# Kernel tuning notes

Measured on AMD Instinct MI355X. Metric: run time of the kernel, lower is better.

## Reference

```python
import jax, jax.numpy as jnp
import numpy as np

EMB = 512
HID = 512
NCLASS = 50257
BATCH = 64
STEPS = 256


def setup_inputs() -> dict:
    key = jax.random.key(0)
    ks = jax.random.split(key, 14)
    s_e = 1.0 / np.sqrt(EMB)
    s_h = 1.0 / np.sqrt(HID)
    inp = {
        "X": jax.random.randint(ks[0], (BATCH, STEPS), 0, NCLASS, dtype=jnp.int32),
        "emb": jax.random.normal(ks[1], (NCLASS, EMB), jnp.float32) * 0.02,
        # layer 1: gates concatenated in order [i, f, g, o]
        "Wi": jax.random.normal(ks[2], (EMB, 4 * HID), jnp.float32) * s_e,
        "Wh": jax.random.normal(ks[3], (HID, 4 * HID), jnp.float32) * s_h,
        "bi": jax.random.normal(ks[4], (4 * HID,), jnp.float32) * 0.01,
        "bh": jax.random.normal(ks[5], (4 * HID,), jnp.float32) * 0.01,
        # layer 2 (computed but unused for the output, as in the original)
        "Wi1": jax.random.normal(ks[6], (HID, 4 * HID), jnp.float32) * s_h,
        "Wh1": jax.random.normal(ks[7], (HID, 4 * HID), jnp.float32) * s_h,
        "bi1": jax.random.normal(ks[8], (4 * HID,), jnp.float32) * 0.01,
        "bh1": jax.random.normal(ks[9], (4 * HID,), jnp.float32) * 0.01,
        # output projection (nn.Linear(n_hidden, n_class, bias=False) => W: [n_class, n_hidden])
        "Wout": jax.random.normal(ks[10], (NCLASS, HID), jnp.float32) * s_h,
        "bout": jnp.ones((NCLASS,), jnp.float32),
    }
    return inp


def _gates(pre):
    i, f, g, o = jnp.split(pre, 4, axis=-1)
    return jax.nn.sigmoid(i), jax.nn.sigmoid(f), jnp.tanh(g), jax.nn.sigmoid(o)


def reference(X, emb, Wi, Wh, bi, bh, Wi1, Wh1, bi1, bh1, Wout, bout):
    x = emb[X]  # [B, T, E]
    B = x.shape[0]
    # precompute input projections for layer 1 for all timesteps: [T, B, 4H]
    xw = jnp.einsum("bte,eh->tbh", x, Wi) + bi + bh

    h0 = jnp.zeros((B, HID), x.dtype)
    carry0 = (h0, h0, h0, h0)  # h, c, h1, c1

    def step(carry, xw_t):
        h, c, h1, c1 = carry
        i, f, g, o = _gates(xw_t + h @ Wh)
        c = f * c + i * g
        h = o * jnp.tanh(c)
        i1, f1, g1, o1 = _gates(h @ Wi1 + bi1 + h1 @ Wh1 + bh1)
        c1 = f1 * c1 + i1 * g1
        h1 = o1 * jnp.tanh(c1)
        return (h, c, h1, c1), None

    (h, c, h1, c1), _ = jax.lax.scan(step, carry0, xw)
    # original: outputs[-1] is layer-1 h at the last timestep
    return h @ Wout.T + bout
```

## Files before the change

### kernel.cpp

```cpp
#include <hip/hip_runtime.h>
#include <cstdint>
#include <cstddef>

#define EMB    512
#define HID    512
#define NCLASS 50257
#define BATCH  64
#define STEPS  256
#define FOURH  2048
#define NBLK   64

typedef __attribute__((ext_vector_type(8))) short    bf16x8;
typedef __attribute__((ext_vector_type(4))) float    f32x4;
typedef __attribute__((ext_vector_type(8))) _Float16 h8v;

__device__ __forceinline__ unsigned short f2bf(float f) {
    union { float f; unsigned int u; } v; v.f = f;
    unsigned int u = v.u;
    return (unsigned short)((u + 0x7fffu + ((u >> 16) & 1u)) >> 16);
}


__global__ void k_bias(const float* __restrict__ bi, const float* __restrict__ bh,
                       float* __restrict__ bias) {
    int i = blockIdx.x * 256 + threadIdx.x;
    if (i < FOURH) bias[i] = bi[i] + bh[i];
}

__global__ void k_wit(const float* __restrict__ Wi, unsigned short* __restrict__ WiT) {
    int n = blockIdx.x;
    int l = threadIdx.x;
    int k0 = l * 8;
    unsigned short t[8];
#pragma unroll
    for (int i = 0; i < 8; i++)
        t[i] = f2bf(Wi[(size_t)(k0 + i) * FOURH + n]);
    uint4 v;
    v.x = (unsigned)t[0] | ((unsigned)t[1] << 16);
    v.y = (unsigned)t[2] | ((unsigned)t[3] << 16);
    v.z = (unsigned)t[4] | ((unsigned)t[5] << 16);
    v.w = (unsigned)t[6] | ((unsigned)t[7] << 16);
    *(uint4*)(WiT + (size_t)n * EMB + k0) = v;
}

__global__ void k_whP(const float* __restrict__ Wh, _Float16* __restrict__ WhP) {
    int idx = blockIdx.x;
    int bidb = idx >> 5, c = idx & 31;
    int ul   = ((c >> 4) << 2) + ((c >> 2) & 3);
    int gate = c & 3;
    int gcol = gate * 512 + bidb * 8 + ul;
    int k0 = threadIdx.x * 8;
    h8v r;
#pragma unroll
    for (int i = 0; i < 8; i++)
        r[i] = (_Float16)Wh[(size_t)(k0 + i) * FOURH + gcol];
    *(h8v*)(WhP + (size_t)idx * 512 + k0) = r;
}

__global__ void k_gather(const int* __restrict__ X, const float* __restrict__ emb,
                         unsigned short* __restrict__ XA) {
    int chunk = blockIdx.x * 256 + threadIdx.x;
    int m  = chunk >> 6;
    int c8 = (chunk & 63) * 8;
    int t = m >> 6, b = m & 63;
    int row = X[b * STEPS + t];
    const float4* src = (const float4*)(emb + (size_t)row * EMB + c8);
    float4 f0 = src[0], f1 = src[1];
    uint4 v;
    v.x = (unsigned)f2bf(f0.x) | ((unsigned)f2bf(f0.y) << 16);
    v.y = (unsigned)f2bf(f0.z) | ((unsigned)f2bf(f0.w) << 16);
    v.z = (unsigned)f2bf(f1.x) | ((unsigned)f2bf(f1.y) << 16);
    v.w = (unsigned)f2bf(f1.z) | ((unsigned)f2bf(f1.w) << 16);
    *(uint4*)(XA + (size_t)m * EMB + c8) = v;
}

__global__ void k_zero(int* __restrict__ p, int n) {
    int i = blockIdx.x * 256 + threadIdx.x;
    if (i < n) p[i] = 0;
}

__global__ __launch_bounds__(256) void k_gemm1(const unsigned short* __restrict__ XA,
                                               const unsigned short* __restrict__ WiT,
                                               const float* __restrict__ bias,
                                               float* __restrict__ XWT) {
    __shared__ unsigned short Al[64 * 48];
    __shared__ unsigned short Bl[64 * 48];
    const int t  = blockIdx.y;
    const int m0 = t * 64;
    const int n0 = blockIdx.x * 64;
    const int tid  = threadIdx.x;
    const int w    = tid >> 6;
    const int lane = tid & 63;
    const int quad = lane >> 4;
    const int l16  = lane & 15;
    const int ar = tid >> 2;
    const int ac = (tid & 3) * 8;

    f32x4 acc[4];
#pragma unroll
    for (int i = 0; i < 4; i++) acc[i] = (f32x4){0.f, 0.f, 0.f, 0.f};

    for (int kk = 0; kk < 16; kk++) {
        const int k0 = kk * 32;
        __syncthreads();
        *(uint4*)(&Al[ar * 48 + ac]) = *(const uint4*)(XA  + (size_t)(m0 + ar) * EMB + k0 + ac);
        *(uint4*)(&Bl[ar * 48 + ac]) = *(const uint4*)(WiT + (size_t)(n0 + ar) * EMB + k0 + ac);
        __syncthreads();
        bf16x8 afrag = *(const bf16x8*)(&Bl[(w * 16 + l16) * 48 + quad * 8]);
#pragma unroll
        for (int mt = 0; mt < 4; mt++) {
            bf16x8 bfrag = *(const bf16x8*)(&Al[(mt * 16 + l16) * 48 + quad * 8]);
            acc[mt] = __builtin_amdgcn_mfma_f32_16x16x32_bf16(afrag, bfrag, acc[mt], 0, 0, 0);
        }
    }
    float bv[4];
#pragma unroll
    for (int r = 0; r < 4; r++) bv[r] = bias[n0 + w * 16 + quad * 4 + r];
#pragma unroll
    for (int mt = 0; mt < 4; mt++)
#pragma unroll
        for (int r = 0; r < 4; r++)
            XWT[((size_t)t * FOURH + n0 + w * 16 + quad * 4 + r) * 64 + mt * 16 + l16]
                = acc[mt][r] + bv[r];
}

__global__ __launch_bounds__(256, 1) void k_rnn(const float* __restrict__ XWT,
                                                const _Float16* __restrict__ WhP,
                                                _Float16* __restrict__ hG,
                                                float* __restrict__ hfinal,
                                                unsigned int* __restrict__ flags) {
    __shared__ _Float16 hw[64 * 8];
    __shared__ unsigned wcnt;

    const int tid  = threadIdx.x;
    const int bid  = blockIdx.x;
    const int lane = tid & 63;
    const int bt   = tid >> 6;
    const int quad = lane >> 4;
    const int l16  = lane & 15;
    const int b    = bt * 16 + l16;

    if (tid == 0) wcnt = 0;
    __syncthreads();

    h8v afrag[2][16];
#pragma unroll
    for (int tt = 0; tt < 2; tt++) {
        const _Float16* wsrc = WhP + ((size_t)(bid * 32 + tt * 16 + l16)) * 512 + quad * 8;
#pragma unroll
        for (int kk = 0; kk < 16; kk++) afrag[tt][kk] = *(const h8v*)(wsrc + kk * 32);
    }

    float c0 = 0.f, c1 = 0.f;
    const size_t xwo0 = (size_t)(bid * 8 + quad) * 64 + b;
    const size_t xwo1 = (size_t)(bid * 8 + 4 + quad) * 64 + b;
    unsigned int* ectr = flags;

    float xwA[4], xwB[4];
#pragma unroll
    for (int g = 0; g < 4; g++) {
        xwA[g] = XWT[(size_t)g * 32768 + xwo0];
        xwB[g] = XWT[(size_t)g * 32768 + xwo1];
    }

    for (int t = 0; t < STEPS; t++) {
        {
            const unsigned tgt = (unsigned)(NBLK * t);
            unsigned guard = 0;
            unsigned v = __hip_atomic_load(ectr, __ATOMIC_RELAXED,
                                           __HIP_MEMORY_SCOPE_AGENT);
            while (v < tgt) {
                __builtin_amdgcn_s_sleep(1);
                if (++guard > (1u << 17)) break;
                v = __hip_atomic_load(ectr, __ATOMIC_RELAXED,
                                      __HIP_MEMORY_SCOPE_AGENT);
            }
        }

        const char* hsrc = (const char*)hG + (size_t)(t & 1) * 65536
                         + (size_t)b * 1024 + quad * 16;
        uint4 qv[16];
#pragma unroll
        for (int kk = 0; kk < 16; kk++)
            asm volatile("global_load_dwordx4 %0, %1, off sc0 sc1"
                         : "=v"(qv[kk]) : "v"(hsrc + kk * 64));
        asm volatile("s_waitcnt vmcnt(0)" ::: "memory");
        __builtin_amdgcn_sched_barrier(0);

        f32x4 aA0 = {0.f,0.f,0.f,0.f}, aA1 = {0.f,0.f,0.f,0.f};
        f32x4 aB0 = {0.f,0.f,0.f,0.f}, aB1 = {0.f,0.f,0.f,0.f};
#pragma unroll
        for (int kk = 0; kk < 16; kk += 2) {
            union { uint4 q; h8v v; } f0, f1;
            f0.q = qv[kk]; f1.q = qv[kk + 1];
            aA0 = __builtin_amdgcn_mfma_f32_16x16x32_f16(afrag[0][kk],     f0.v, aA0, 0, 0, 0);
            aB0 = __builtin_amdgcn_mfma_f32_16x16x32_f16(afrag[1][kk],     f0.v, aB0, 0, 0, 0);
            aA1 = __builtin_amdgcn_mfma_f32_16x16x32_f16(afrag[0][kk + 1], f1.v, aA1, 0, 0, 0);
            aB1 = __builtin_amdgcn_mfma_f32_16x16x32_f16(afrag[1][kk + 1], f1.v, aB1, 0, 0, 0);
        }
        f32x4 accA = aA0 + aA1;
        f32x4 accB = aB0 + aB1;

        float iA = 1.f / (1.f + __expf(-(accA[0] + xwA[0])));
        float fA = 1.f / (1.f + __expf(-(accA[1] + xwA[1])));
        float gA = tanhf(accA[2] + xwA[2]);
        float oA = 1.f / (1.f + __expf(-(accA[3] + xwA[3])));
        c0 = fA * c0 + iA * gA;
        float hnA = oA * tanhf(c0);

        float iB = 1.f / (1.f + __expf(-(accB[0] + xwB[0])));
        float fB = 1.f / (1.f + __expf(-(accB[1] + xwB[1])));
        float gB = tanhf(accB[2] + xwB[2]);
        float oB = 1.f / (1.f + __expf(-(accB[3] + xwB[3])));
        c1 = fB * c1 + iB * gB;
        float hnB = oB * tanhf(c1);

        if (t == STEPS - 1) {
            hfinal[(size_t)b * HID + bid * 8 + quad]     = hnA;
            hfinal[(size_t)b * HID + bid * 8 + 4 + quad] = hnB;
            break;
        }

        hw[b * 8 + quad]     = (_Float16)hnA;
        hw[b * 8 + 4 + quad] = (_Float16)hnB;
        asm volatile("s_waitcnt lgkmcnt(0)" ::: "memory");
        if (quad == 0) {
            const unsigned long long* src = (const unsigned long long*)(hw + b * 8);
            unsigned long long lo = src[0], hi = src[1];
            unsigned long long* dst = (unsigned long long*)((char*)hG
                + (size_t)((t + 1) & 1) * 65536 + (size_t)b * 1024 + bid * 16);
            __hip_atomic_store(dst,     lo, __ATOMIC_RELAXED, __HIP_MEMORY_SCOPE_AGENT);
            __hip_atomic_store(dst + 1, hi, __ATOMIC_RELAXED, __HIP_MEMORY_SCOPE_AGENT);
        }
        asm volatile("s_waitcnt vmcnt(0)" ::: "memory");
        if (lane == 0) {
            unsigned old = atomicAdd(&wcnt, 1u);
            if (old == (unsigned)(4 * t + 3))
                __hip_atomic_fetch_add(ectr, 1u, __ATOMIC_RELAXED,
                                       __HIP_MEMORY_SCOPE_AGENT);
        }

        {
            const float* xp = XWT + (size_t)(t + 1) * (FOURH * 64);
#pragma unroll
            for (int g = 0; g < 4; g++) {
                xwA[g] = xp[(size_t)g * 32768 + xwo0];
                xwB[g] = xp[(size_t)g * 32768 + xwo1];
            }
            asm volatile("" :: "v"(xwA[0]), "v"(xwA[1]), "v"(xwA[2]), "v"(xwA[3]),
                              "v"(xwB[0]), "v"(xwB[1]), "v"(xwB[2]), "v"(xwB[3]));
        }
    }
}

__global__ __launch_bounds__(128) void k_out(const float* __restrict__ Wout,
                                             const float* __restrict__ bout,
                                             const float* __restrict__ hfinal,
                                             float* __restrict__ out) {
    __shared__ float hl[BATCH * 128];
    const int tid = threadIdx.x;
    const int n = blockIdx.x * 128 + tid;
    const bool valid = n < NCLASS;
    float acc[BATCH];
#pragma unroll
    for (int b = 0; b < BATCH; b++) acc[b] = 0.f;
    const float4* W4 = (const float4*)Wout;
    const float4* h4 = (const float4*)hfinal;
    float4* hl4 = (float4*)hl;

    for (int kq = 0; kq < 4; kq++) {
        __syncthreads();
#pragma unroll
        for (int i = 0; i < 16; i++) {
            int f = i * 128 + tid;
            int b = f >> 5, kk = f & 31;
            hl4[f] = h4[b * 128 + kq * 32 + kk];
        }
        __syncthreads();
        if (valid) {
            for (int kk = 0; kk < 32; kk++) {
                float4 wv = W4[(size_t)n * 128 + kq * 32 + kk];
#pragma unroll
                for (int b = 0; b < BATCH; b++) {
                    float4 hv = hl4[b * 32 + kk];
                    acc[b] = fmaf(wv.x, hv.x, acc[b]);
                    acc[b] = fmaf(wv.y, hv.y, acc[b]);
                    acc[b] = fmaf(wv.z, hv.z, acc[b]);
                    acc[b] = fmaf(wv.w, hv.w, acc[b]);
                }
            }
        }
    }
    if (valid) {
        float bv = bout[n];
        for (int b = 0; b < BATCH; b++)
            out[(size_t)b * NCLASS + n] = acc[b] + bv;
    }
}


extern "C" void kernel_launch(void* const* d_in, const int* in_sizes, int n_in,
                              void* d_out, int out_size, void* d_ws, size_t ws_size,
                              hipStream_t stream) {
    const int*   X    = (const int*)  d_in[0];
    const float* emb  = (const float*)d_in[1];
    const float* Wi   = (const float*)d_in[2];
    const float* Wh   = (const float*)d_in[3];
    const float* bi   = (const float*)d_in[4];
    const float* bh   = (const float*)d_in[5];
    const float* Wout = (const float*)d_in[10];
    const float* bout = (const float*)d_in[11];
    float* out = (float*)d_out;

    char* w = (char*)d_ws;
    float*          XWT    = (float*)(w);
    unsigned short* XA     = (unsigned short*)(w + 134217728);
    _Float16*       hG     = (_Float16*)(w + 150732800);
    unsigned int*   flags  = (unsigned int*)(w + 150863872);
    unsigned short* WiT    = (unsigned short*)(w + 150994944);
    _Float16*       WhP    = (_Float16*)(w + 153092096);
    float*          bias   = (float*)(w + 155189248);
    float*          hfinal = (float*)(w + 155197440);

    k_bias  <<<8,    256, 0, stream>>>(bi, bh, bias);
    k_wit   <<<2048,  64, 0, stream>>>(Wi, WiT);
    k_whP   <<<2048,  64, 0, stream>>>(Wh, WhP);
    k_gather<<<4096, 256, 0, stream>>>(X, emb, XA);
    k_gemm1 <<<dim3(32, 256), 256, 0, stream>>>(XA, WiT, bias, XWT);
    k_zero  <<<132,  256, 0, stream>>>((int*)hG, 33792);

    k_rnn   <<<NBLK, 256, 0, stream>>>(XWT, WhP, hG, hfinal, flags);

    k_out   <<<393,  128, 0, stream>>>(Wout, bout, hfinal, out);
}
```

Before: 1.877 ms.

## Replace global atomic counter barrier with per-block flags polled by one wave

The grid-wide step barrier used to be a single shared atomic counter that every wave polled. Now each block writes its own step number to a padded per-block flag, and only wave 0 polls all 64 flags in parallel (one per lane) using a wave-wide all-vote. The other waves spin on an LDS epoch variable. This removes atomic contention on one cache line and cuts global polling traffic, at the cost of a two-level wait and relaxed-ordering assumptions around the LDS handoff.

```diff
diff --git a/kernel.cpp b/kernel.cpp
--- a/kernel.cpp
+++ b/kernel.cpp
@@ -131,6 +131,7 @@
                                                 unsigned int* __restrict__ flags) {
     __shared__ _Float16 hw[64 * 8];
     __shared__ unsigned wcnt;
+    __shared__ int      ep;
 
     const int tid  = threadIdx.x;
     const int bid  = blockIdx.x;
@@ -140,7 +141,7 @@
     const int l16  = lane & 15;
     const int b    = bt * 16 + l16;
 
-    if (tid == 0) wcnt = 0;
+    if (tid == 0) { wcnt = 0; ep = 0; }
     __syncthreads();
 
     h8v afrag[2][16];
@@ -154,7 +155,6 @@
     float c0 = 0.f, c1 = 0.f;
     const size_t xwo0 = (size_t)(bid * 8 + quad) * 64 + b;
     const size_t xwo1 = (size_t)(bid * 8 + 4 + quad) * 64 + b;
-    unsigned int* ectr = flags;
 
     float xwA[4], xwB[4];
 #pragma unroll
@@ -164,16 +164,25 @@
     }
 
     for (int t = 0; t < STEPS; t++) {
-        {
-            const unsigned tgt = (unsigned)(NBLK * t);
-            unsigned guard = 0;
-            unsigned v = __hip_atomic_load(ectr, __ATOMIC_RELAXED,
-                                           __HIP_MEMORY_SCOPE_AGENT);
-            while (v < tgt) {
-                __builtin_amdgcn_s_sleep(1);
-                if (++guard > (1u << 17)) break;
-                v = __hip_atomic_load(ectr, __ATOMIC_RELAXED,
-                                      __HIP_MEMORY_SCOPE_AGENT);
+        if (t > 0) {
+            if (bt == 0) {
+                const unsigned tgt = (unsigned)t;
+                unsigned guard = 0;
+                unsigned v = __hip_atomic_load(&flags[lane * 16],
+                                               __ATOMIC_RELAXED, __HIP_MEMORY_SCOPE_AGENT);
+                while (!__all(v >= tgt)) {
+                    __builtin_amdgcn_s_sleep(1);
+                    if (++guard > (1u << 17)) break;
+                    v = __hip_atomic_load(&flags[lane * 16],
+                                          __ATOMIC_RELAXED, __HIP_MEMORY_SCOPE_AGENT);
+                }
+                if (lane == 0) *(volatile int*)&ep = t;
+            } else {
+                unsigned guard = 0;
+                while (*(volatile int*)&ep < t) {
+                    __builtin_amdgcn_s_sleep(1);
+                    if (++guard > (1u << 20)) break;
+                }
             }
         }
 
@@ -236,8 +245,8 @@
         if (lane == 0) {
             unsigned old = atomicAdd(&wcnt, 1u);
             if (old == (unsigned)(4 * t + 3))
-                __hip_atomic_fetch_add(ectr, 1u, __ATOMIC_RELAXED,
-                                       __HIP_MEMORY_SCOPE_AGENT);
+                __hip_atomic_store(&flags[bid * 16], (unsigned)(t + 1),
+                                   __ATOMIC_RELAXED, __HIP_MEMORY_SCOPE_AGENT);
         }
 
         {
```

Result: faster. 1.641 ms (-12.6%).
